# Optimization experiments

Measured on AMD Instinct MI355X. Metric: run time of the kernel, lower is better.

The kernel has to match this reference:

```python
import jax, jax.numpy as jnp
import numpy as np

NUM_USERS = 200000
NUM_ITEMS = 100000
DIM = 64
NUM_LAYERS = 2
NUM_EDGES = 3200000
EPS = 1e-12  # F.normalize eps


def setup_inputs() -> dict:
    key = jax.random.key(0)
    ks = jax.random.split(key, 8)
    return {
        "user_emb": jax.random.normal(ks[0], (NUM_USERS, DIM), dtype=jnp.float32),
        "item_emb": jax.random.normal(ks[1], (NUM_ITEMS, DIM), dtype=jnp.float32),
        "Wu": jax.random.normal(ks[2], (NUM_LAYERS, DIM, 2 * DIM), dtype=jnp.float32) * 0.1,
        "Wi": jax.random.normal(ks[3], (NUM_LAYERS, DIM, 2 * DIM), dtype=jnp.float32) * 0.1,
        "u_idx": jax.random.randint(ks[4], (NUM_EDGES,), 0, NUM_USERS, dtype=jnp.int32),
        "i_idx": jax.random.randint(ks[5], (NUM_EDGES,), 0, NUM_ITEMS, dtype=jnp.int32),
        "w_u2i": jax.random.uniform(ks[6], (NUM_EDGES,), dtype=jnp.float32),
        "w_i2u": jax.random.uniform(ks[7], (NUM_EDGES,), dtype=jnp.float32),
    }


def _l2_normalize(x):
    # matches F.normalize(p=2, dim=1): x / max(||x||, eps)
    n = jnp.sqrt(jnp.sum(x * x, axis=1, keepdims=True))
    return x / jnp.maximum(n, EPS)


def _spmm(vals, rows, cols, h, num_rows):
    # (sparse [num_rows, num_cols]) @ h : gather rows of h at cols, scale, scatter-add
    msg = vals[:, None] * h[cols]  # [E, DIM]
    return jax.ops.segment_sum(msg, rows, num_segments=num_rows)


def reference(user_emb, item_emb, Wu, Wi, u_idx, i_idx, w_u2i, w_i2u):
    h_u, h_i = user_emb, item_emb
    for l in range(NUM_LAYERS):
        neigh_u = _spmm(w_u2i, u_idx, i_idx, h_i, NUM_USERS)   # adj_u2i @ h_i
        neigh_i = _spmm(w_i2u, i_idx, u_idx, h_u, NUM_ITEMS)   # adj_i2u @ h_u
        # Linear(2*dim -> dim, no bias): concat then x @ W.T
        h_u_new = jax.nn.relu(jnp.concatenate([h_u, neigh_u], axis=1) @ Wu[l].T)
        h_i_new = jax.nn.relu(jnp.concatenate([h_i, neigh_i], axis=1) @ Wi[l].T)
        h_u = _l2_normalize(h_u_new)
        h_i = _l2_normalize(h_i_new)
    return (h_u, h_i)
```

## Files before the change

kernel.cpp:

```cpp
#include <hip/hip_runtime.h>


#define N_USERS 200000
#define N_ITEMS 100000
#define N_EDGES 3200000
#define NB_U 782
#define NB_I 391

__global__ __launch_bounds__(256) void wprep_kernel(
    const float* __restrict__ Wu, const float* __restrict__ Wi,
    float* __restrict__ WuT, float* __restrict__ WiT)
{
    int idx = blockIdx.x * 256 + threadIdx.x;
    const float* src = Wu;
    float* dst = WuT;
    int i = idx;
    if (idx >= 16384) { src = Wi; dst = WiT; i = idx - 16384; }
    int l = i >> 13;
    int r = i & 8191;
    int j = r >> 7;
    int k = r & 127;
    dst[l * 8192 + k * 64 + j] = src[i];
}

__global__ __launch_bounds__(256) void hist_kernel(
    const int* __restrict__ u_idx, const int* __restrict__ i_idx,
    int* __restrict__ deg_u, int* __restrict__ deg_i,
    unsigned short* __restrict__ rank_u, unsigned short* __restrict__ rank_i)
{
    int t = blockIdx.x * 256 + threadIdx.x;
    if (t < N_EDGES) {
        rank_u[t] = (unsigned short)atomicAdd(&deg_u[u_idx[t]], 1);
    } else {
        int e = t - N_EDGES;
        rank_i[e] = (unsigned short)atomicAdd(&deg_i[i_idx[e]], 1);
    }
}

__global__ __launch_bounds__(256) void scanA_kernel(
    const int* __restrict__ deg_u, const int* __restrict__ deg_i,
    int* __restrict__ bsum_u, int* __restrict__ bsum_i)
{
    int b = blockIdx.x;
    const int* deg; int n; int* bs; int bb;
    if (b < NB_U) { deg = deg_u; n = N_USERS; bs = bsum_u; bb = b; }
    else          { deg = deg_i; n = N_ITEMS; bs = bsum_i; bb = b - NB_U; }
    int i = bb * 256 + threadIdx.x;
    int v = (i < n) ? deg[i] : 0;
    #pragma unroll
    for (int off = 1; off < 64; off <<= 1) v += __shfl_xor(v, off);
    __shared__ int ws4[4];
    int wv = threadIdx.x >> 6;
    if ((threadIdx.x & 63) == 0) ws4[wv] = v;
    __syncthreads();
    if (threadIdx.x == 0) bs[bb] = ws4[0] + ws4[1] + ws4[2] + ws4[3];
}

__global__ __launch_bounds__(1024) void scanB_kernel(
    const int* __restrict__ bsum_u, int* __restrict__ bpre_u,
    const int* __restrict__ bsum_i, int* __restrict__ bpre_i)
{
    __shared__ int s[1024];
    const int* src; int* dst; int n;
    if (blockIdx.x == 0) { src = bsum_u; dst = bpre_u; n = NB_U; }
    else                 { src = bsum_i; dst = bpre_i; n = NB_I; }
    int t = threadIdx.x;
    int v = (t < n) ? src[t] : 0;
    s[t] = v; __syncthreads();
    #pragma unroll
    for (int off = 1; off < 1024; off <<= 1) {
        int x = (t >= off) ? s[t - off] : 0;
        __syncthreads();
        s[t] += x;
        __syncthreads();
    }
    if (t < n) dst[t] = s[t] - v;
}

__global__ __launch_bounds__(256) void scanC_kernel(
    const int* __restrict__ deg_u, const int* __restrict__ deg_i,
    const int* __restrict__ bpre_u, const int* __restrict__ bpre_i,
    int* __restrict__ rowptr_u, int* __restrict__ rowptr_i)
{
    int b = blockIdx.x;
    const int* deg; int n; const int* bpre; int* rowptr; int bb;
    if (b < NB_U) { deg = deg_u; n = N_USERS; bpre = bpre_u; rowptr = rowptr_u; bb = b; }
    else          { deg = deg_i; n = N_ITEMS; bpre = bpre_i; rowptr = rowptr_i; bb = b - NB_U; }
    int t = threadIdx.x;
    int i = bb * 256 + t;
    int d = (i < n) ? deg[i] : 0;
    __shared__ int s[256];
    s[t] = d; __syncthreads();
    #pragma unroll
    for (int off = 1; off < 256; off <<= 1) {
        int x = (t >= off) ? s[t - off] : 0;
        __syncthreads();
        s[t] += x;
        __syncthreads();
    }
    int val = bpre[bb] + (s[t] - d);
    if (i < n) rowptr[i] = val;
    if (b == 0 && t == 0) { rowptr_u[N_USERS] = N_EDGES; rowptr_i[N_ITEMS] = N_EDGES; }
}

__global__ __launch_bounds__(256) void fill_kernel(
    const int* __restrict__ u_idx, const int* __restrict__ i_idx,
    const float* __restrict__ w_u2i, const float* __restrict__ w_i2u,
    const unsigned short* __restrict__ rank_u, const unsigned short* __restrict__ rank_i,
    const int* __restrict__ rowptr_u, const int* __restrict__ rowptr_i,
    uint2* __restrict__ edges_u, uint2* __restrict__ edges_i)
{
    const int part   = blockIdx.x & 7;
    const int slot   = blockIdx.x >> 3;
    const int nslots = gridDim.x >> 3;
    const int stride = nslots * 256;

    for (int e = slot * 256 + threadIdx.x; e < N_EDGES; e += stride) {
        int ru = u_idx[e];
        int ri = i_idx[e];
        if ((ru & 7) == part) {
            int p = rowptr_u[ru] + rank_u[e];
            edges_u[p] = make_uint2((unsigned)ri, __float_as_uint(w_u2i[e]));
        }
        if ((ri & 7) == part) {
            int p = rowptr_i[ri] + rank_i[e];
            edges_i[p] = make_uint2((unsigned)ru, __float_as_uint(w_i2u[e]));
        }
    }
}

__global__ __launch_bounds__(256, 4) void transform_fused_kernel(
    const float* __restrict__ hself, const float* __restrict__ hsrc,
    const int* __restrict__ rowptr, const uint2* __restrict__ edges,
    const float* __restrict__ Wt, float* __restrict__ out, int N)
{
    __shared__ float Ws[64 * 64];
    __shared__ float Xs[64 * 68];

    const int tid  = threadIdx.x;
    const int row0 = blockIdx.x * 64;

    #pragma unroll
    for (int i = 0; i < 16; ++i) Ws[tid + i * 256] = Wt[tid + i * 256];
    #pragma unroll
    for (int i = 0; i < 16; ++i) {
        int idx = tid + i * 256;
        int rr = idx >> 6, cc = idx & 63;
        int gr = row0 + rr; if (gr > N - 1) gr = N - 1;
        Xs[rr * 68 + cc] = hself[gr * 64 + cc];
    }
    __syncthreads();

    const int tr = tid >> 3;
    const int tc = tid & 7;
    const int r0 = 2 * tr;

    float acc[2][8];
    #pragma unroll
    for (int j = 0; j < 2; ++j)
        #pragma unroll
        for (int c = 0; c < 8; ++c) acc[j][c] = 0.f;

    #pragma unroll 8
    for (int k = 0; k < 64; ++k) {
        float a0 = Xs[r0 * 68 + k];
        float a1 = Xs[(r0 + 1) * 68 + k];
        float4 b0 = *(const float4*)&Ws[k * 64 + 8 * tc];
        float4 b1 = *(const float4*)&Ws[k * 64 + 8 * tc + 4];
        float b[8] = {b0.x, b0.y, b0.z, b0.w, b1.x, b1.y, b1.z, b1.w};
        #pragma unroll
        for (int c = 0; c < 8; ++c) {
            acc[0][c] = fmaf(a0, b[c], acc[0][c]);
            acc[1][c] = fmaf(a1, b[c], acc[1][c]);
        }
    }
    __syncthreads();

    {
        const float4* src = (const float4*)(Wt + 4096);
        float4* dst = (float4*)Ws;
        #pragma unroll
        for (int i = 0; i < 4; ++i) dst[tid + i * 256] = src[tid + i * 256];
    }

    {
        const int wv = tid >> 6;
        const int ln = tid & 63;
        #pragma unroll 1
        for (int half = 0; half < 2; ++half) {
            const int rbase = row0 + wv * 16 + half * 8;
            int   ecur[8], eend[8];
            float gacc[8];
            #pragma unroll
            for (int rl = 0; rl < 8; ++rl) {
                int r = rbase + rl;
                if (r < N) { ecur[rl] = rowptr[r]; eend[rl] = rowptr[r + 1]; }
                else       { ecur[rl] = 0;         eend[rl] = 0; }
                gacc[rl] = 0.f;
            }
            int dmax = 0;
            #pragma unroll
            for (int rl = 0; rl < 8; ++rl) dmax = max(dmax, eend[rl] - ecur[rl]);

            uint2 ec[8];
            #pragma unroll
            for (int rl = 0; rl < 8; ++rl)
                ec[rl] = edges[min(ecur[rl], N_EDGES - 1)];

            #pragma unroll 1
            for (int it = 0; it < dmax; ++it) {
                float hv[8], wg[8];
                #pragma unroll
                for (int rl = 0; rl < 8; ++rl) {
                    bool v = ecur[rl] < eend[rl];
                    wg[rl] = v ? __uint_as_float(ec[rl].y) : 0.f;
                    hv[rl] = hsrc[(int)ec[rl].x * 64 + ln];
                    ecur[rl] += v ? 1 : 0;
                }
                #pragma unroll
                for (int rl = 0; rl < 8; ++rl)
                    ec[rl] = edges[min(ecur[rl], N_EDGES - 1)];
                #pragma unroll
                for (int rl = 0; rl < 8; ++rl)
                    gacc[rl] = fmaf(wg[rl], hv[rl], gacc[rl]);
            }
            #pragma unroll
            for (int rl = 0; rl < 8; ++rl)
                Xs[(wv * 16 + half * 8 + rl) * 68 + ln] = gacc[rl];
        }
    }
    __syncthreads();

    #pragma unroll 8
    for (int k = 0; k < 64; ++k) {
        float a0 = Xs[r0 * 68 + k];
        float a1 = Xs[(r0 + 1) * 68 + k];
        float4 b0 = *(const float4*)&Ws[k * 64 + 8 * tc];
        float4 b1 = *(const float4*)&Ws[k * 64 + 8 * tc + 4];
        float b[8] = {b0.x, b0.y, b0.z, b0.w, b1.x, b1.y, b1.z, b1.w};
        #pragma unroll
        for (int c = 0; c < 8; ++c) {
            acc[0][c] = fmaf(a0, b[c], acc[0][c]);
            acc[1][c] = fmaf(a1, b[c], acc[1][c]);
        }
    }

    #pragma unroll
    for (int j = 0; j < 2; ++j) {
        float s = 0.f;
        #pragma unroll
        for (int c = 0; c < 8; ++c) {
            float v = fmaxf(acc[j][c], 0.f);
            acc[j][c] = v;
            s = fmaf(v, v, s);
        }
        s += __shfl_xor(s, 1);
        s += __shfl_xor(s, 2);
        s += __shfl_xor(s, 4);
        float nrm = sqrtf(s);
        float inv = 1.f / fmaxf(nrm, 1e-12f);
        int gr = row0 + r0 + j;
        if (gr < N) {
            float4 o0 = make_float4(acc[j][0]*inv, acc[j][1]*inv, acc[j][2]*inv, acc[j][3]*inv);
            float4 o1 = make_float4(acc[j][4]*inv, acc[j][5]*inv, acc[j][6]*inv, acc[j][7]*inv);
            float* p = out + gr * 64 + 8 * tc;
            *(float4*)p       = o0;
            *(float4*)(p + 4) = o1;
        }
    }
}

extern "C" void kernel_launch(void* const* d_in, const int* in_sizes, int n_in,
                              void* d_out, int out_size, void* d_ws, size_t ws_size,
                              hipStream_t stream)
{
    (void)in_sizes; (void)n_in; (void)out_size; (void)ws_size;

    const float* user_emb = (const float*)d_in[0];
    const float* item_emb = (const float*)d_in[1];
    const float* Wu       = (const float*)d_in[2];
    const float* Wi       = (const float*)d_in[3];
    const int*   u_idx    = (const int*)d_in[4];
    const int*   i_idx    = (const int*)d_in[5];
    const float* w_u2i    = (const float*)d_in[6];
    const float* w_i2u    = (const float*)d_in[7];
    float* out = (float*)d_out;

    float* ws      = (float*)d_ws;
    float* WuT     = ws;
    float* WiT     = WuT + 16384;
    float* hu1     = WiT + 16384;
    float* hi1     = hu1 + N_USERS * 64;
    uint2* edges_u = (uint2*)(hi1 + N_ITEMS * 64);
    uint2* edges_i = edges_u + N_EDGES;
    unsigned short* rank_u = (unsigned short*)(edges_i + N_EDGES);
    unsigned short* rank_i = rank_u + N_EDGES;
    int* rowptr_u = (int*)(rank_i + N_EDGES);
    int* rowptr_i = rowptr_u + (N_USERS + 1);
    int* deg_u    = rowptr_i + (N_ITEMS + 1);
    int* deg_i    = deg_u + N_USERS;
    int* bsum_u   = deg_i + N_ITEMS;
    int* bpre_u   = bsum_u + NB_U;
    int* bsum_i   = bpre_u + NB_U;
    int* bpre_i   = bsum_i + NB_I;

    const int tu_blocks = (N_USERS + 63) / 64;
    const int ti_blocks = (N_ITEMS + 63) / 64;
    const int e2_blocks = (2 * N_EDGES) / 256;

    wprep_kernel<<<128, 256, 0, stream>>>(Wu, Wi, WuT, WiT);
    hipMemsetAsync(deg_u, 0, (size_t)(N_USERS + N_ITEMS) * 4, stream);
    hist_kernel<<<e2_blocks, 256, 0, stream>>>(u_idx, i_idx, deg_u, deg_i, rank_u, rank_i);
    scanA_kernel<<<NB_U + NB_I, 256, 0, stream>>>(deg_u, deg_i, bsum_u, bsum_i);
    scanB_kernel<<<2, 1024, 0, stream>>>(bsum_u, bpre_u, bsum_i, bpre_i);
    scanC_kernel<<<NB_U + NB_I, 256, 0, stream>>>(deg_u, deg_i, bpre_u, bpre_i, rowptr_u, rowptr_i);
    fill_kernel<<<2048, 256, 0, stream>>>(u_idx, i_idx, w_u2i, w_i2u,
                                          rank_u, rank_i, rowptr_u, rowptr_i,
                                          edges_u, edges_i);

    transform_fused_kernel<<<tu_blocks, 256, 0, stream>>>(user_emb, item_emb, rowptr_u, edges_u, WuT, hu1, N_USERS);
    transform_fused_kernel<<<ti_blocks, 256, 0, stream>>>(item_emb, user_emb, rowptr_i, edges_i, WiT, hi1, N_ITEMS);

    transform_fused_kernel<<<tu_blocks, 256, 0, stream>>>(hu1, hi1, rowptr_u, edges_u, WuT + 8192, out, N_USERS);
    transform_fused_kernel<<<ti_blocks, 256, 0, stream>>>(hi1, hu1, rowptr_i, edges_i, WiT + 8192, out + (size_t)N_USERS * 64, N_ITEMS);
}
```

Before: 1.489 ms.

## Balance SpMM gather by splitting block edges evenly and merge user/item launches

```diff
diff --git a/kernel.cpp b/kernel.cpp
--- a/kernel.cpp
+++ b/kernel.cpp
@@ -130,15 +130,30 @@
 }
 
 __global__ __launch_bounds__(256, 4) void transform_fused_kernel(
-    const float* __restrict__ hself, const float* __restrict__ hsrc,
-    const int* __restrict__ rowptr, const uint2* __restrict__ edges,
-    const float* __restrict__ Wt, float* __restrict__ out, int N)
+    const float* __restrict__ hself_u, const float* __restrict__ hsrc_u,
+    const int* __restrict__ rowptr_u, const uint2* __restrict__ edges_u,
+    const float* __restrict__ WtU, float* __restrict__ out_u,
+    const float* __restrict__ hself_i, const float* __restrict__ hsrc_i,
+    const int* __restrict__ rowptr_i, const uint2* __restrict__ edges_i,
+    const float* __restrict__ WtI, float* __restrict__ out_i,
+    int nbu)
 {
     __shared__ float Ws[64 * 64];
     __shared__ float Xs[64 * 68];
-
-    const int tid  = threadIdx.x;
-    const int row0 = blockIdx.x * 64;
+    __shared__ int   rp_s[65];
+
+    const int tid = threadIdx.x;
+
+    const float* hself; const float* hsrc; const int* rowptr;
+    const uint2* edges; const float* Wt; float* out; int N; int bb;
+    if ((int)blockIdx.x < nbu) {
+        hself = hself_u; hsrc = hsrc_u; rowptr = rowptr_u; edges = edges_u;
+        Wt = WtU; out = out_u; N = N_USERS; bb = blockIdx.x;
+    } else {
+        hself = hself_i; hsrc = hsrc_i; rowptr = rowptr_i; edges = edges_i;
+        Wt = WtI; out = out_i; N = N_ITEMS; bb = blockIdx.x - nbu;
+    }
+    const int row0 = bb * 64;
 
     #pragma unroll
     for (int i = 0; i < 16; ++i) Ws[tid + i * 256] = Wt[tid + i * 256];
@@ -149,6 +164,7 @@
         int gr = row0 + rr; if (gr > N - 1) gr = N - 1;
         Xs[rr * 68 + cc] = hself[gr * 64 + cc];
     }
+    if (tid <= 64) rp_s[tid] = rowptr[min(row0 + tid, N)];
     __syncthreads();
 
     const int tr = tid >> 3;
@@ -181,52 +197,67 @@
         float4* dst = (float4*)Ws;
         #pragma unroll
         for (int i = 0; i < 4; ++i) dst[tid + i * 256] = src[tid + i * 256];
-    }
+        #pragma unroll
+        for (int i = 0; i < 17; ++i) Xs[tid + i * 256] = 0.f;
+    }
+    __syncthreads();
 
     {
         const int wv = tid >> 6;
         const int ln = tid & 63;
+        const int e0 = rp_s[0], e1 = rp_s[64];
+        const int perw = (e1 - e0 + 3) >> 2;
+        const int wsb  = e0 + wv * perw;
+        const int web  = min(wsb + perw, e1);
+        const int clen = (web - wsb + 7) >> 3;
+
+        int   cs[8], ce[8], rr[8], nend[8];
+        float gacc[8];
+        uint2 ec[8];
+        #pragma unroll
+        for (int c = 0; c < 8; ++c) {
+            cs[c] = wsb + c * clen;
+            ce[c] = min(cs[c] + clen, web);
+            gacc[c] = 0.f;
+            int lo = 0, hi = 64;
+            #pragma unroll
+            for (int s = 0; s < 6; ++s) {
+                int mid = (lo + hi) >> 1;
+                bool go = rp_s[mid] <= cs[c];
+                lo = go ? mid : lo;
+                hi = go ? hi : mid;
+            }
+            rr[c] = lo; nend[c] = rp_s[lo + 1];
+            ec[c] = edges[min(cs[c], N_EDGES - 1)];
+        }
+
         #pragma unroll 1
-        for (int half = 0; half < 2; ++half) {
-            const int rbase = row0 + wv * 16 + half * 8;
-            int   ecur[8], eend[8];
-            float gacc[8];
+        for (int it = 0; it < clen; ++it) {
+            float hv[8], wg[8];
             #pragma unroll
-            for (int rl = 0; rl < 8; ++rl) {
-                int r = rbase + rl;
-                if (r < N) { ecur[rl] = rowptr[r]; eend[rl] = rowptr[r + 1]; }
-                else       { ecur[rl] = 0;         eend[rl] = 0; }
-                gacc[rl] = 0.f;
-            }
-            int dmax = 0;
-            #pragma unroll
-            for (int rl = 0; rl < 8; ++rl) dmax = max(dmax, eend[rl] - ecur[rl]);
-
-            uint2 ec[8];
-            #pragma unroll
-            for (int rl = 0; rl < 8; ++rl)
-                ec[rl] = edges[min(ecur[rl], N_EDGES - 1)];
-
-            #pragma unroll 1
-            for (int it = 0; it < dmax; ++it) {
-                float hv[8], wg[8];
-                #pragma unroll
-                for (int rl = 0; rl < 8; ++rl) {
-                    bool v = ecur[rl] < eend[rl];
-                    wg[rl] = v ? __uint_as_float(ec[rl].y) : 0.f;
-                    hv[rl] = hsrc[(int)ec[rl].x * 64 + ln];
-                    ecur[rl] += v ? 1 : 0;
-                }
-                #pragma unroll
-                for (int rl = 0; rl < 8; ++rl)
-                    ec[rl] = edges[min(ecur[rl], N_EDGES - 1)];
-                #pragma unroll
-                for (int rl = 0; rl < 8; ++rl)
-                    gacc[rl] = fmaf(wg[rl], hv[rl], gacc[rl]);
+            for (int c = 0; c < 8; ++c) {
+                bool v = (cs[c] + it) < ce[c];
+                wg[c] = v ? __uint_as_float(ec[c].y) : 0.f;
+                hv[c] = hsrc[(int)ec[c].x * 64 + ln];
             }
             #pragma unroll
-            for (int rl = 0; rl < 8; ++rl)
-                Xs[(wv * 16 + half * 8 + rl) * 68 + ln] = gacc[rl];
+            for (int c = 0; c < 8; ++c)
+                ec[c] = edges[min(cs[c] + it + 1, N_EDGES - 1)];
+            #pragma unroll
+            for (int c = 0; c < 8; ++c) {
+                gacc[c] = fmaf(wg[c], hv[c], gacc[c]);
+                int p   = cs[c] + it;
+                int nxt = p + 1;
+                if (p < ce[c] && (nxt == nend[c] || nxt == ce[c])) {
+                    atomicAdd(&Xs[rr[c] * 68 + ln], gacc[c]);
+                    gacc[c] = 0.f;
+                    if (nxt == nend[c] && nxt < web) {
+                        int r2 = rr[c];
+                        while (r2 < 63 && rp_s[r2 + 1] <= nxt) ++r2;
+                        rr[c] = r2; nend[c] = rp_s[r2 + 1];
+                    }
+                }
+            }
         }
     }
     __syncthreads();
@@ -318,9 +349,11 @@
                                           rank_u, rank_i, rowptr_u, rowptr_i,
                                           edges_u, edges_i);
 
-    transform_fused_kernel<<<tu_blocks, 256, 0, stream>>>(user_emb, item_emb, rowptr_u, edges_u, WuT, hu1, N_USERS);
-    transform_fused_kernel<<<ti_blocks, 256, 0, stream>>>(item_emb, user_emb, rowptr_i, edges_i, WiT, hi1, N_ITEMS);
-
-    transform_fused_kernel<<<tu_blocks, 256, 0, stream>>>(hu1, hi1, rowptr_u, edges_u, WuT + 8192, out, N_USERS);
-    transform_fused_kernel<<<ti_blocks, 256, 0, stream>>>(hi1, hu1, rowptr_i, edges_i, WiT + 8192, out + (size_t)N_USERS * 64, N_ITEMS);
-}
+    transform_fused_kernel<<<tu_blocks + ti_blocks, 256, 0, stream>>>(
+        user_emb, item_emb, rowptr_u, edges_u, WuT, hu1,
+        item_emb, user_emb, rowptr_i, edges_i, WiT, hi1, tu_blocks);
+
+    transform_fused_kernel<<<tu_blocks + ti_blocks, 256, 0, stream>>>(
+        hu1, hi1, rowptr_u, edges_u, WuT + 8192, out,
+        hi1, hu1, rowptr_i, edges_i, WiT + 8192, out + (size_t)N_USERS * 64, tu_blocks);
+}
```

After: 1.348 ms. 9.5% less time.
